# Performance work log

Hardware: AMD Instinct MI355X
Metric: run time of the kernel (lower is better)

The kernel has to match this reference:

```python
import jax, jax.numpy as jnp
import numpy as np

N, E, F_IN, HID, EMB, G = 100000, 1600000, 128, 128, 128, 64


def setup_inputs() -> dict:
    key = jax.random.key(0)
    ks = jax.random.split(key, 8)
    x = jax.random.normal(ks[0], (N, F_IN), jnp.float32)
    edge_index = jax.random.randint(ks[1], (2, E), 0, N, dtype=jnp.int64)
    batch = jnp.sort(jax.random.randint(ks[2], (N,), 0, G, dtype=jnp.int64))
    s1 = 1.0 / np.sqrt(F_IN)
    s2 = 1.0 / np.sqrt(HID)
    W1 = jax.random.uniform(ks[3], (F_IN, HID), jnp.float32, -s1, s1)
    b1 = jnp.zeros((HID,), jnp.float32)
    W2 = jax.random.uniform(ks[4], (HID, HID), jnp.float32, -s2, s2)
    b2 = jnp.zeros((HID,), jnp.float32)
    Wp = jax.random.uniform(ks[5], (HID, EMB), jnp.float32, -s2, s2)
    bp = jax.random.uniform(ks[6], (EMB,), jnp.float32, -s2, s2)
    return dict(x=x, edge_index=edge_index, batch=batch,
                W1=W1, b1=b1, W2=W2, b2=b2, Wp=Wp, bp=bp)


def _gcn_norm(edge_index, num_nodes):
    # PyG GCNConv: add self-loops, symmetric normalization D^-1/2 (A+I) D^-1/2
    loops = jnp.arange(num_nodes, dtype=edge_index.dtype)
    row = jnp.concatenate([edge_index[0], loops])  # sources
    col = jnp.concatenate([edge_index[1], loops])  # targets
    deg = jax.ops.segment_sum(jnp.ones_like(col, jnp.float32), col, num_segments=num_nodes)
    dis = jnp.where(deg > 0, jax.lax.rsqrt(jnp.maximum(deg, 1.0)), 0.0)
    norm = dis[row] * dis[col]  # [E + N]
    return row, col, norm


def reference(x, edge_index, batch, W1, b1, W2, b2, Wp, bp):
    n = x.shape[0]
    row, col, norm = _gcn_norm(edge_index, n)

    def gcn(h, W, b):
        h = h @ W                                   # [N, HID] small GEMM
        msg = h[row] * norm[:, None]                # gather + scale [E+N, HID]
        return jax.ops.segment_sum(msg, col, num_segments=n) + b  # scatter-add

    h = jax.nn.relu(gcn(x, W1, b1))   # dropout p=0.2 is identity in eval mode
    h = jax.nn.relu(gcn(h, W2, b2))
    # global_mean_pool over graph ids
    cnt = jax.ops.segment_sum(jnp.ones((n,), jnp.float32), batch, num_segments=G)
    pooled = jax.ops.segment_sum(h, batch, num_segments=G) / jnp.maximum(cnt, 1.0)[:, None]
    return pooled @ Wp + bp  # [G, EMB]
```

## Files before the change

### kernel.cpp

```cpp
#include <hip/hip_runtime.h>
#include <cstdint>
#include <cstddef>

#define GG 64
#define EPB 4096
#define BUK_SHIFT 9
#define BUK_NODES 512
#define PCHUNK 64

typedef unsigned int uint;
typedef unsigned short ushort;
typedef __attribute__((ext_vector_type(8))) short short8v;
typedef __attribute__((ext_vector_type(4))) float f32x4;


__global__ __launch_bounds__(256) void hist_kernel(const int* __restrict__ col,
                                                   int* __restrict__ ghist,
                                                   int E, int nbuk) {
  __shared__ int h[256];
  const int tid = threadIdx.x;
  h[tid] = 0;
  __syncthreads();
  const int base = blockIdx.x * EPB;
#pragma unroll
  for (int j = 0; j < EPB / 256; ++j) {
    int e = base + j * 256 + tid;
    if (e < E) atomicAdd(&h[col[e] >> BUK_SHIFT], 1);
  }
  __syncthreads();
  if (tid < nbuk && h[tid]) atomicAdd(&ghist[tid], h[tid]);
}

__global__ __launch_bounds__(256) void scan_kernel(const int* __restrict__ ghist,
                                                   int* __restrict__ bucketBase,
                                                   int* __restrict__ gcur,
                                                   int nbuk, int E) {
  __shared__ int s[256];
  const int tid = threadIdx.x;
  int v = (tid < nbuk) ? ghist[tid] : 0;
  s[tid] = v;
  __syncthreads();
  for (int off = 1; off < 256; off <<= 1) {
    int t = 0;
    if (tid >= off) t = s[tid - off];
    __syncthreads();
    s[tid] += t;
    __syncthreads();
  }
  int excl = s[tid] - v;
  if (tid < nbuk) {
    bucketBase[tid] = excl;
    gcur[tid] = excl;
  }
  if (tid == 0) bucketBase[nbuk] = E;
}

__global__ __launch_bounds__(256) void bin_kernel(const int* __restrict__ row,
                                                  const int* __restrict__ col,
                                                  int* __restrict__ gcur,
                                                  uint* __restrict__ binned, int E) {
  __shared__ int h[256];
  __shared__ int bbase[256];
  __shared__ int lcur[256];
  const int tid = threadIdx.x;
  const int base = blockIdx.x * EPB;
  int src[EPB / 256];
  int dst[EPB / 256];
#pragma unroll
  for (int j = 0; j < EPB / 256; ++j) {
    int e = base + j * 256 + tid;
    if (e < E) {
      src[j] = row[e];
      dst[j] = col[e];
    } else {
      dst[j] = -1;
    }
  }
  h[tid] = 0;
  lcur[tid] = 0;
  __syncthreads();
#pragma unroll
  for (int j = 0; j < EPB / 256; ++j)
    if (dst[j] >= 0) atomicAdd(&h[dst[j] >> BUK_SHIFT], 1);
  __syncthreads();
  if (h[tid] > 0) bbase[tid] = atomicAdd(&gcur[tid], h[tid]);
  __syncthreads();
#pragma unroll
  for (int j = 0; j < EPB / 256; ++j) {
    if (dst[j] >= 0) {
      int b = dst[j] >> BUK_SHIFT;
      int r = atomicAdd(&lcur[b], 1);
      binned[bbase[b] + r] = (uint)src[j] | ((uint)(dst[j] & (BUK_NODES - 1)) << 17);
    }
  }
}

__global__ __launch_bounds__(256) void build_kernel(const uint* __restrict__ binned,
                                                    const int* __restrict__ bucketBase,
                                                    int* __restrict__ indptr,
                                                    float* __restrict__ dis,
                                                    int* __restrict__ csr,
                                                    int n, int E, int nbuk) {
  __shared__ int h[BUK_NODES];
  __shared__ int off[BUK_NODES];
  __shared__ int ps[256];
  const int tid = threadIdx.x;
  const int b = blockIdx.x;
  const int lo = bucketBase[b], hi = bucketBase[b + 1];
  h[tid] = 0;
  h[tid + 256] = 0;
  __syncthreads();
  for (int i = lo + tid; i < hi; i += 256) atomicAdd(&h[binned[i] >> 17], 1);
  __syncthreads();
  int a0 = h[2 * tid], a1 = h[2 * tid + 1];
  ps[tid] = a0 + a1;
  __syncthreads();
  for (int o = 1; o < 256; o <<= 1) {
    int t = 0;
    if (tid >= o) t = ps[tid - o];
    __syncthreads();
    ps[tid] += t;
    __syncthreads();
  }
  int pexcl = ps[tid] - (a0 + a1);
  off[2 * tid] = pexcl;
  off[2 * tid + 1] = pexcl + a0;
  __syncthreads();
  const int node0 = b << BUK_SHIFT;
#pragma unroll
  for (int k = tid; k < BUK_NODES; k += 256) {
    int node = node0 + k;
    if (node < n) {
      indptr[node] = lo + off[k];
      dis[node] = rsqrtf((float)(h[k] + 1));
    }
  }
  __syncthreads();
  for (int i = lo + tid; i < hi; i += 256) {
    uint u = binned[i];
    int dlow = u >> 17;
    int s = (int)(u & 0x1FFFFu);
    int r = atomicAdd(&off[dlow], 1);
    csr[lo + r] = s;
  }
  if (b == nbuk - 1 && tid == 0) indptr[n] = E;
}


__device__ __forceinline__ uint bf16rne(float f) {
  uint u = __float_as_uint(f);
  return (u + 0x7fffu + ((u >> 16) & 1u)) >> 16;
}

__global__ __launch_bounds__(256) void wconv_kernel(const float* __restrict__ W,
                                                    ushort* __restrict__ Whi,
                                                    ushort* __restrict__ Wlo) {
  int slot = blockIdx.x * 256 + threadIdx.x;
  if (slot >= 2048) return;
  int lane = slot & 63;
  int j = (slot >> 6) & 7;
  int kc = slot >> 9;
  ushort hb[8], lb[8];
#pragma unroll
  for (int i = 0; i < 8; ++i) {
    int k = kc * 32 + ((lane >> 4) << 3) + i;
    int c = j * 16 + (lane & 15);
    float f = W[k * 128 + c];
    uint hi = bf16rne(f);
    float hif = __uint_as_float(hi << 16);
    uint lo = __float_as_uint(f - hif) >> 16;
    hb[i] = (ushort)hi;
    lb[i] = (ushort)lo;
  }
  *reinterpret_cast<uint4*>(Whi + (size_t)slot * 8) = *reinterpret_cast<uint4*>(hb);
  *reinterpret_cast<uint4*>(Wlo + (size_t)slot * 8) = *reinterpret_cast<uint4*>(lb);
}


__global__ __launch_bounds__(256) void gemm_mfma(const float* __restrict__ A,
                                                 const ushort* __restrict__ Whi,
                                                 const ushort* __restrict__ Wlo,
                                                 const float* __restrict__ scale,
                                                 uint* __restrict__ Cb, int n) {
  const int tid = threadIdx.x;
  const int wave = tid >> 6, lane = tid & 63;
  const int row = blockIdx.x * 64 + wave * 16 + (lane & 15);
  const int kgrp = lane >> 4;
  const bool rowok = row < n;

  f32x4 acc[8];
#pragma unroll
  for (int j = 0; j < 8; ++j) acc[j] = (f32x4){0.f, 0.f, 0.f, 0.f};

#pragma unroll
  for (int kc = 0; kc < 4; ++kc) {
    const float* ap = A + (size_t)row * 128 + kc * 32 + kgrp * 8;
    float4 a0 = make_float4(0.f, 0.f, 0.f, 0.f), a1 = a0;
    if (rowok) {
      a0 = *reinterpret_cast<const float4*>(ap);
      a1 = *reinterpret_cast<const float4*>(ap + 4);
    }
    short8v ahi, alo;
#pragma unroll
    for (int i = 0; i < 8; ++i) {
      float f = (i < 4) ? (&a0.x)[i] : (&a1.x)[i - 4];
      uint hi = bf16rne(f);
      float hif = __uint_as_float(hi << 16);
      uint lo = __float_as_uint(f - hif) >> 16;
      ahi[i] = (short)hi;
      alo[i] = (short)lo;
    }
#pragma unroll
    for (int j = 0; j < 8; ++j) {
      const size_t base = ((size_t)(kc * 8 + j) * 64 + lane) * 8;
      short8v whi = *reinterpret_cast<const short8v*>(Whi + base);
      short8v wlo = *reinterpret_cast<const short8v*>(Wlo + base);
      acc[j] = __builtin_amdgcn_mfma_f32_16x16x32_bf16(whi, ahi, acc[j], 0, 0, 0);
      acc[j] = __builtin_amdgcn_mfma_f32_16x16x32_bf16(whi, alo, acc[j], 0, 0, 0);
      acc[j] = __builtin_amdgcn_mfma_f32_16x16x32_bf16(wlo, ahi, acc[j], 0, 0, 0);
    }
  }

  if (rowok) {
    const float s = scale[row];
#pragma unroll
    for (int j = 0; j < 8; ++j) {
      uint u0 = bf16rne(acc[j][0] * s) | (bf16rne(acc[j][1] * s) << 16);
      uint u1 = bf16rne(acc[j][2] * s) | (bf16rne(acc[j][3] * s) << 16);
      *reinterpret_cast<uint2*>(Cb + (size_t)row * 64 + j * 8 + kgrp * 2) =
          make_uint2(u0, u1);
    }
  }
}


__global__ __launch_bounds__(256) void agg_kernel(const uint* __restrict__ T,
                                                  const int* __restrict__ indptr,
                                                  const int* __restrict__ csr,
                                                  const float* __restrict__ dis,
                                                  const float* __restrict__ bias,
                                                  float* __restrict__ O, int n) {
  int wid = (blockIdx.x << 2) + (threadIdx.x >> 6);
  if (wid >= n) return;
  wid = __builtin_amdgcn_readfirstlane(wid);
  const int lane = threadIdx.x & 63;
  const int e0 = indptr[wid], e1 = indptr[wid + 1];
  float ax = 0.f, ay = 0.f;
#define TLOAD(s) T[(size_t)(s) * 64 + lane]
#define BLO(u) __uint_as_float((u) << 16)
#define BHI(u) __uint_as_float((u) & 0xffff0000u)
  int e = e0;
  for (; e + 8 <= e1; e += 8) {
    int s0 = csr[e], s1 = csr[e + 1], s2 = csr[e + 2], s3 = csr[e + 3];
    int s4 = csr[e + 4], s5 = csr[e + 5], s6 = csr[e + 6], s7 = csr[e + 7];
    uint u0 = TLOAD(s0), u1 = TLOAD(s1), u2 = TLOAD(s2), u3 = TLOAD(s3);
    uint u4 = TLOAD(s4), u5 = TLOAD(s5), u6 = TLOAD(s6), u7 = TLOAD(s7);
    ax += ((BLO(u0) + BLO(u1)) + (BLO(u2) + BLO(u3))) +
          ((BLO(u4) + BLO(u5)) + (BLO(u6) + BLO(u7)));
    ay += ((BHI(u0) + BHI(u1)) + (BHI(u2) + BHI(u3))) +
          ((BHI(u4) + BHI(u5)) + (BHI(u6) + BHI(u7)));
  }
  for (; e + 4 <= e1; e += 4) {
    int s0 = csr[e], s1 = csr[e + 1], s2 = csr[e + 2], s3 = csr[e + 3];
    uint u0 = TLOAD(s0), u1 = TLOAD(s1), u2 = TLOAD(s2), u3 = TLOAD(s3);
    ax += (BLO(u0) + BLO(u1)) + (BLO(u2) + BLO(u3));
    ay += (BHI(u0) + BHI(u1)) + (BHI(u2) + BHI(u3));
  }
  for (; e < e1; ++e) {
    uint u = TLOAD(csr[e]);
    ax += BLO(u);
    ay += BHI(u);
  }
  uint us = TLOAD(wid);
  ax += BLO(us);
  ay += BHI(us);
  const float di = dis[wid];
  const float2 b = *reinterpret_cast<const float2*>(bias + lane * 2);
  float ox = fmaxf(fmaf(di, ax, b.x), 0.f);
  float oy = fmaxf(fmaf(di, ay, b.y), 0.f);
  *reinterpret_cast<float2*>(O + (size_t)wid * 128 + lane * 2) = make_float2(ox, oy);
}


__global__ __launch_bounds__(256) void pool_kernel(const float* __restrict__ H,
                                                   const int* __restrict__ batch,
                                                   float* __restrict__ pooled,
                                                   float* __restrict__ cntg, int n) {
  __shared__ float sd[256 * 4];
  const int tid = threadIdx.x;
  const int c4 = (tid & 31) << 2;
  const int rs = tid >> 5;
  const int base = blockIdx.x * PCHUNK;
  const int lim = min(base + PCHUNK, n);
  const int g0 = batch[base];
  const int gN = batch[lim - 1];
  float4 acc = make_float4(0.f, 0.f, 0.f, 0.f);
  if (g0 == gN) {
    for (int r = base + rs; r < lim; r += 8) {
      float4 v = *reinterpret_cast<const float4*>(H + (size_t)r * 128 + c4);
      acc.x += v.x; acc.y += v.y; acc.z += v.z; acc.w += v.w;
    }
    *reinterpret_cast<float4*>(&sd[tid * 4]) = acc;
    __syncthreads();
    if (tid < 128) {
      float4 o = *reinterpret_cast<float4*>(&sd[(tid + 128) * 4]);
      acc.x += o.x; acc.y += o.y; acc.z += o.z; acc.w += o.w;
      *reinterpret_cast<float4*>(&sd[tid * 4]) = acc;
    }
    __syncthreads();
    if (tid < 64) {
      float4 o = *reinterpret_cast<float4*>(&sd[(tid + 64) * 4]);
      acc.x += o.x; acc.y += o.y; acc.z += o.z; acc.w += o.w;
      *reinterpret_cast<float4*>(&sd[tid * 4]) = acc;
    }
    __syncthreads();
    if (tid < 32) {
      float4 o = *reinterpret_cast<float4*>(&sd[(tid + 32) * 4]);
      acc.x += o.x; acc.y += o.y; acc.z += o.z; acc.w += o.w;
      atomicAdd(&pooled[g0 * 128 + c4 + 0], acc.x);
      atomicAdd(&pooled[g0 * 128 + c4 + 1], acc.y);
      atomicAdd(&pooled[g0 * 128 + c4 + 2], acc.z);
      atomicAdd(&pooled[g0 * 128 + c4 + 3], acc.w);
      if (tid == 0) atomicAdd(&cntg[g0], (float)(lim - base));
    }
  } else {
    int curg = -1, cnt = 0;
    for (int r = base + rs; r < lim; r += 8) {
      int g = batch[r];
      if (g != curg) {
        if (curg >= 0) {
          atomicAdd(&pooled[curg * 128 + c4 + 0], acc.x);
          atomicAdd(&pooled[curg * 128 + c4 + 1], acc.y);
          atomicAdd(&pooled[curg * 128 + c4 + 2], acc.z);
          atomicAdd(&pooled[curg * 128 + c4 + 3], acc.w);
          if ((tid & 31) == 0) atomicAdd(&cntg[curg], (float)cnt);
        }
        curg = g;
        acc = make_float4(0.f, 0.f, 0.f, 0.f);
        cnt = 0;
      }
      float4 v = *reinterpret_cast<const float4*>(H + (size_t)r * 128 + c4);
      acc.x += v.x; acc.y += v.y; acc.z += v.z; acc.w += v.w;
      cnt++;
    }
    if (curg >= 0) {
      atomicAdd(&pooled[curg * 128 + c4 + 0], acc.x);
      atomicAdd(&pooled[curg * 128 + c4 + 1], acc.y);
      atomicAdd(&pooled[curg * 128 + c4 + 2], acc.z);
      atomicAdd(&pooled[curg * 128 + c4 + 3], acc.w);
      if ((tid & 31) == 0) atomicAdd(&cntg[curg], (float)cnt);
    }
  }
}

__global__ __launch_bounds__(128) void final_kernel(const float* __restrict__ pooled,
                                                    const float* __restrict__ cntg,
                                                    const float* __restrict__ Wp,
                                                    const float* __restrict__ bp,
                                                    float* __restrict__ out) {
  const int g = blockIdx.x;
  const int e = threadIdx.x;
  float inv = 1.0f / fmaxf(cntg[g], 1.0f);
  float acc = 0.f;
  for (int c = 0; c < 128; ++c)
    acc = fmaf(pooled[g * 128 + c], Wp[c * 128 + e], acc);
  out[g * 128 + e] = acc * inv + bp[e];
}


extern "C" void kernel_launch(void* const* d_in, const int* in_sizes, int n_in,
                              void* d_out, int out_size, void* d_ws, size_t ws_size,
                              hipStream_t stream) {
  const float* x = (const float*)d_in[0];
  const int* eidx = (const int*)d_in[1];
  const int* batch = (const int*)d_in[2];
  const float* W1 = (const float*)d_in[3];
  const float* b1 = (const float*)d_in[4];
  const float* W2 = (const float*)d_in[5];
  const float* b2 = (const float*)d_in[6];
  const float* Wp = (const float*)d_in[7];
  const float* bp = (const float*)d_in[8];

  const int n = in_sizes[0] / 128;
  const int E = in_sizes[1] / 2;
  const int* row = eidx;
  const int* col = eidx + E;
  const int nbuk = (n + BUK_NODES - 1) >> BUK_SHIFT;

  char* ws = (char*)d_ws;
  size_t off = 0;
  auto alloc = [&](size_t bytes) {
    void* p = ws + off;
    off = (off + bytes + 255) & ~(size_t)255;
    return p;
  };
  uint* Tb = (uint*)alloc((size_t)n * 64 * 4);
  float* B = (float*)alloc((size_t)n * 128 * 4);
  float* dis = (float*)alloc((size_t)n * 4);
  int* indptr = (int*)alloc((size_t)(n + 1) * 4);
  int* csr = (int*)alloc((size_t)E * 4);
  uint* binned = (uint*)alloc((size_t)E * 4);
  int* ghist = (int*)alloc(256 * 4);
  int* bucketBase = (int*)alloc(257 * 4);
  int* gcur = (int*)alloc(256 * 4);
  float* pooled = (float*)alloc((size_t)GG * 128 * 4);
  float* cntg = (float*)alloc((size_t)GG * 4);
  ushort* Whi1 = (ushort*)alloc(2048 * 8 * 2);
  ushort* Wlo1 = (ushort*)alloc(2048 * 8 * 2);
  ushort* Whi2 = (ushort*)alloc(2048 * 8 * 2);
  ushort* Wlo2 = (ushort*)alloc(2048 * 8 * 2);
  (void)off;

  hipMemsetAsync(ghist, 0, 256 * 4, stream);
  hipMemsetAsync(pooled, 0, (size_t)GG * 128 * 4, stream);
  hipMemsetAsync(cntg, 0, (size_t)GG * 4, stream);

  const int eblocks = (E + EPB - 1) / EPB;
  hist_kernel<<<eblocks, 256, 0, stream>>>(col, ghist, E, nbuk);
  scan_kernel<<<1, 256, 0, stream>>>(ghist, bucketBase, gcur, nbuk, E);
  bin_kernel<<<eblocks, 256, 0, stream>>>(row, col, gcur, binned, E);
  build_kernel<<<nbuk, 256, 0, stream>>>(binned, bucketBase, indptr, dis, csr, n, E, nbuk);
  wconv_kernel<<<8, 256, 0, stream>>>(W1, Whi1, Wlo1);
  wconv_kernel<<<8, 256, 0, stream>>>(W2, Whi2, Wlo2);

  const int gblocks = (n + 63) / 64;
  gemm_mfma<<<gblocks, 256, 0, stream>>>(x, Whi1, Wlo1, dis, Tb, n);
  agg_kernel<<<(n + 3) / 4, 256, 0, stream>>>(Tb, indptr, csr, dis, b1, B, n);
  gemm_mfma<<<gblocks, 256, 0, stream>>>(B, Whi2, Wlo2, dis, Tb, n);
  agg_kernel<<<(n + 3) / 4, 256, 0, stream>>>(Tb, indptr, csr, dis, b2, B, n);

  pool_kernel<<<(n + PCHUNK - 1) / PCHUNK, 256, 0, stream>>>(B, batch, pooled, cntg, n);
  final_kernel<<<GG, 128, 0, stream>>>(pooled, cntg, Wp, bp, (float*)d_out);
}
```

Before: 287.5 us.

## Store hidden activations in bf16, sub-bucket CSR by source, merge setup launches

The aggregation output is now written as packed bf16 instead of fp32. The second GEMM reads bf16 activations directly and drops one of its three split-precision MFMAs, and the pool kernel reads the halved data. The CSR build now sorts each destination's edges into 8 sub-bins keyed by the high bits of the source id, for better gather locality in aggregation, and it stores an expanded indptr. The two weight-conversion launches and three memsets are each merged into one. This lowers memory traffic and launch count but rounds the intermediate activations to bf16, which reduces accuracy.

```diff
diff --git a/kernel.cpp b/kernel.cpp
--- a/kernel.cpp
+++ b/kernel.cpp
@@ -7,11 +7,20 @@
 #define BUK_SHIFT 9
 #define BUK_NODES 512
 #define PCHUNK 64
+#define NCH 8
 
 typedef unsigned int uint;
 typedef unsigned short ushort;
 typedef __attribute__((ext_vector_type(8))) short short8v;
 typedef __attribute__((ext_vector_type(4))) float f32x4;
+
+__device__ __forceinline__ float blo(uint u) { return __uint_as_float(u << 16); }
+__device__ __forceinline__ float bhi(uint u) { return __uint_as_float(u & 0xffff0000u); }
+
+__device__ __forceinline__ uint bf16rne(float f) {
+  uint u = __float_as_uint(f);
+  return (u + 0x7fffu + ((u >> 16) & 1u)) >> 16;
+}
 
 
 __global__ __launch_bounds__(256) void hist_kernel(const int* __restrict__ col,
@@ -97,23 +106,34 @@
 
 __global__ __launch_bounds__(256) void build_kernel(const uint* __restrict__ binned,
                                                     const int* __restrict__ bucketBase,
-                                                    int* __restrict__ indptr,
+                                                    int* __restrict__ ip2,
                                                     float* __restrict__ dis,
                                                     int* __restrict__ csr,
                                                     int n, int E, int nbuk) {
-  __shared__ int h[BUK_NODES];
-  __shared__ int off[BUK_NODES];
+  __shared__ int h[BUK_NODES * NCH];
+  __shared__ int off[BUK_NODES * NCH];
   __shared__ int ps[256];
   const int tid = threadIdx.x;
   const int b = blockIdx.x;
   const int lo = bucketBase[b], hi = bucketBase[b + 1];
-  h[tid] = 0;
-  h[tid + 256] = 0;
-  __syncthreads();
-  for (int i = lo + tid; i < hi; i += 256) atomicAdd(&h[binned[i] >> 17], 1);
-  __syncthreads();
-  int a0 = h[2 * tid], a1 = h[2 * tid + 1];
-  ps[tid] = a0 + a1;
+#pragma unroll
+  for (int k = tid; k < BUK_NODES * NCH; k += 256) h[k] = 0;
+  __syncthreads();
+  for (int i = lo + tid; i < hi; i += 256) {
+    uint u = binned[i];
+    int key = (int)((u >> 17) << 3) | (int)((u & 0x1FFFFu) >> 14);
+    atomicAdd(&h[key], 1);
+  }
+  __syncthreads();
+  const int b16 = tid * 16;
+  int loc[16];
+  int s = 0;
+#pragma unroll
+  for (int j = 0; j < 16; ++j) {
+    loc[j] = s;
+    s += h[b16 + j];
+  }
+  ps[tid] = s;
   __syncthreads();
   for (int o = 1; o < 256; o <<= 1) {
     int t = 0;
@@ -122,41 +142,45 @@
     ps[tid] += t;
     __syncthreads();
   }
-  int pexcl = ps[tid] - (a0 + a1);
-  off[2 * tid] = pexcl;
-  off[2 * tid + 1] = pexcl + a0;
+  const int excl = ps[tid] - s;
+#pragma unroll
+  for (int j = 0; j < 16; ++j) off[b16 + j] = excl + loc[j];
   __syncthreads();
   const int node0 = b << BUK_SHIFT;
-#pragma unroll
   for (int k = tid; k < BUK_NODES; k += 256) {
     int node = node0 + k;
     if (node < n) {
-      indptr[node] = lo + off[k];
-      dis[node] = rsqrtf((float)(h[k] + 1));
+      int deg = 0;
+#pragma unroll
+      for (int c = 0; c < NCH; ++c) deg += h[k * NCH + c];
+      dis[node] = rsqrtf((float)(deg + 1));
+#pragma unroll
+      for (int c = 0; c < NCH; ++c) ip2[(size_t)node * NCH + c] = lo + off[k * NCH + c];
     }
   }
   __syncthreads();
   for (int i = lo + tid; i < hi; i += 256) {
     uint u = binned[i];
-    int dlow = u >> 17;
-    int s = (int)(u & 0x1FFFFu);
-    int r = atomicAdd(&off[dlow], 1);
-    csr[lo + r] = s;
-  }
-  if (b == nbuk - 1 && tid == 0) indptr[n] = E;
-}
-
-
-__device__ __forceinline__ uint bf16rne(float f) {
-  uint u = __float_as_uint(f);
-  return (u + 0x7fffu + ((u >> 16) & 1u)) >> 16;
-}
-
-__global__ __launch_bounds__(256) void wconv_kernel(const float* __restrict__ W,
-                                                    ushort* __restrict__ Whi,
-                                                    ushort* __restrict__ Wlo) {
-  int slot = blockIdx.x * 256 + threadIdx.x;
-  if (slot >= 2048) return;
+    int key = (int)((u >> 17) << 3) | (int)((u & 0x1FFFFu) >> 14);
+    int s2 = (int)(u & 0x1FFFFu);
+    int r = atomicAdd(&off[key], 1);
+    csr[lo + r] = s2;
+  }
+  if (b == nbuk - 1 && tid == 0) ip2[(size_t)n * NCH] = E;
+}
+
+
+__global__ __launch_bounds__(256) void wconv_kernel(const float* __restrict__ W1,
+                                                    const float* __restrict__ W2,
+                                                    ushort* __restrict__ Whi1,
+                                                    ushort* __restrict__ Wlo1,
+                                                    ushort* __restrict__ Whi2,
+                                                    ushort* __restrict__ Wlo2) {
+  const int g = blockIdx.x;
+  const float* W = (g < 8) ? W1 : W2;
+  ushort* Whi = (g < 8) ? Whi1 : Whi2;
+  ushort* Wlo = (g < 8) ? Wlo1 : Wlo2;
+  int slot = (g & 7) * 256 + threadIdx.x;
   int lane = slot & 63;
   int j = (slot >> 6) & 7;
   int kc = slot >> 9;
@@ -177,7 +201,8 @@
 }
 
 
-__global__ __launch_bounds__(256) void gemm_mfma(const float* __restrict__ A,
+template <bool ABF16>
+__global__ __launch_bounds__(256) void gemm_mfma(const void* __restrict__ Ain,
                                                  const ushort* __restrict__ Whi,
                                                  const ushort* __restrict__ Wlo,
                                                  const float* __restrict__ scale,
@@ -194,21 +219,31 @@
 
 #pragma unroll
   for (int kc = 0; kc < 4; ++kc) {
-    const float* ap = A + (size_t)row * 128 + kc * 32 + kgrp * 8;
-    float4 a0 = make_float4(0.f, 0.f, 0.f, 0.f), a1 = a0;
-    if (rowok) {
-      a0 = *reinterpret_cast<const float4*>(ap);
-      a1 = *reinterpret_cast<const float4*>(ap + 4);
-    }
     short8v ahi, alo;
-#pragma unroll
-    for (int i = 0; i < 8; ++i) {
-      float f = (i < 4) ? (&a0.x)[i] : (&a1.x)[i - 4];
-      uint hi = bf16rne(f);
-      float hif = __uint_as_float(hi << 16);
-      uint lo = __float_as_uint(f - hif) >> 16;
-      ahi[i] = (short)hi;
-      alo[i] = (short)lo;
+    if constexpr (ABF16) {
+      if (rowok) {
+        ahi = *reinterpret_cast<const short8v*>(
+            (const ushort*)Ain + (size_t)row * 128 + kc * 32 + kgrp * 8);
+      } else {
+#pragma unroll
+        for (int i = 0; i < 8; ++i) ahi[i] = 0;
+      }
+    } else {
+      const float* ap = (const float*)Ain + (size_t)row * 128 + kc * 32 + kgrp * 8;
+      float4 a0 = make_float4(0.f, 0.f, 0.f, 0.f), a1 = a0;
+      if (rowok) {
+        a0 = *reinterpret_cast<const float4*>(ap);
+        a1 = *reinterpret_cast<const float4*>(ap + 4);
+      }
+#pragma unroll
+      for (int i = 0; i < 8; ++i) {
+        float f = (i < 4) ? (&a0.x)[i] : (&a1.x)[i - 4];
+        uint hi = bf16rne(f);
+        float hif = __uint_as_float(hi << 16);
+        uint lo = __float_as_uint(f - hif) >> 16;
+        ahi[i] = (short)hi;
+        alo[i] = (short)lo;
+      }
     }
 #pragma unroll
     for (int j = 0; j < 8; ++j) {
@@ -216,7 +251,8 @@
       short8v whi = *reinterpret_cast<const short8v*>(Whi + base);
       short8v wlo = *reinterpret_cast<const short8v*>(Wlo + base);
       acc[j] = __builtin_amdgcn_mfma_f32_16x16x32_bf16(whi, ahi, acc[j], 0, 0, 0);
-      acc[j] = __builtin_amdgcn_mfma_f32_16x16x32_bf16(whi, alo, acc[j], 0, 0, 0);
+      if constexpr (!ABF16)
+        acc[j] = __builtin_amdgcn_mfma_f32_16x16x32_bf16(whi, alo, acc[j], 0, 0, 0);
       acc[j] = __builtin_amdgcn_mfma_f32_16x16x32_bf16(wlo, ahi, acc[j], 0, 0, 0);
     }
   }
@@ -235,54 +271,53 @@
 
 
 __global__ __launch_bounds__(256) void agg_kernel(const uint* __restrict__ T,
-                                                  const int* __restrict__ indptr,
+                                                  const int* __restrict__ ip2,
                                                   const int* __restrict__ csr,
                                                   const float* __restrict__ dis,
                                                   const float* __restrict__ bias,
-                                                  float* __restrict__ O, int n) {
+                                                  uint* __restrict__ O, int n) {
   int wid = (blockIdx.x << 2) + (threadIdx.x >> 6);
   if (wid >= n) return;
   wid = __builtin_amdgcn_readfirstlane(wid);
   const int lane = threadIdx.x & 63;
-  const int e0 = indptr[wid], e1 = indptr[wid + 1];
+  const int e0 = ip2[(size_t)wid * NCH];
+  const int e1 = ip2[(size_t)wid * NCH + NCH];
   float ax = 0.f, ay = 0.f;
 #define TLOAD(s) T[(size_t)(s) * 64 + lane]
-#define BLO(u) __uint_as_float((u) << 16)
-#define BHI(u) __uint_as_float((u) & 0xffff0000u)
   int e = e0;
   for (; e + 8 <= e1; e += 8) {
     int s0 = csr[e], s1 = csr[e + 1], s2 = csr[e + 2], s3 = csr[e + 3];
     int s4 = csr[e + 4], s5 = csr[e + 5], s6 = csr[e + 6], s7 = csr[e + 7];
     uint u0 = TLOAD(s0), u1 = TLOAD(s1), u2 = TLOAD(s2), u3 = TLOAD(s3);
     uint u4 = TLOAD(s4), u5 = TLOAD(s5), u6 = TLOAD(s6), u7 = TLOAD(s7);
-    ax += ((BLO(u0) + BLO(u1)) + (BLO(u2) + BLO(u3))) +
-          ((BLO(u4) + BLO(u5)) + (BLO(u6) + BLO(u7)));
-    ay += ((BHI(u0) + BHI(u1)) + (BHI(u2) + BHI(u3))) +
-          ((BHI(u4) + BHI(u5)) + (BHI(u6) + BHI(u7)));
+    ax += ((blo(u0) + blo(u1)) + (blo(u2) + blo(u3))) +
+          ((blo(u4) + blo(u5)) + (blo(u6) + blo(u7)));
+    ay += ((bhi(u0) + bhi(u1)) + (bhi(u2) + bhi(u3))) +
+          ((bhi(u4) + bhi(u5)) + (bhi(u6) + bhi(u7)));
   }
   for (; e + 4 <= e1; e += 4) {
     int s0 = csr[e], s1 = csr[e + 1], s2 = csr[e + 2], s3 = csr[e + 3];
     uint u0 = TLOAD(s0), u1 = TLOAD(s1), u2 = TLOAD(s2), u3 = TLOAD(s3);
-    ax += (BLO(u0) + BLO(u1)) + (BLO(u2) + BLO(u3));
-    ay += (BHI(u0) + BHI(u1)) + (BHI(u2) + BHI(u3));
+    ax += (blo(u0) + blo(u1)) + (blo(u2) + blo(u3));
+    ay += (bhi(u0) + bhi(u1)) + (bhi(u2) + bhi(u3));
   }
   for (; e < e1; ++e) {
     uint u = TLOAD(csr[e]);
-    ax += BLO(u);
-    ay += BHI(u);
+    ax += blo(u);
+    ay += bhi(u);
   }
   uint us = TLOAD(wid);
-  ax += BLO(us);
-  ay += BHI(us);
+  ax += blo(us);
+  ay += bhi(us);
   const float di = dis[wid];
   const float2 b = *reinterpret_cast<const float2*>(bias + lane * 2);
   float ox = fmaxf(fmaf(di, ax, b.x), 0.f);
   float oy = fmaxf(fmaf(di, ay, b.y), 0.f);
-  *reinterpret_cast<float2*>(O + (size_t)wid * 128 + lane * 2) = make_float2(ox, oy);
-}
-
-
-__global__ __launch_bounds__(256) void pool_kernel(const float* __restrict__ H,
+  O[(size_t)wid * 64 + lane] = bf16rne(ox) | (bf16rne(oy) << 16);
+}
+
+
+__global__ __launch_bounds__(256) void pool_kernel(const uint* __restrict__ H,
                                                    const int* __restrict__ batch,
                                                    float* __restrict__ pooled,
                                                    float* __restrict__ cntg, int n) {
@@ -297,8 +332,8 @@
   float4 acc = make_float4(0.f, 0.f, 0.f, 0.f);
   if (g0 == gN) {
     for (int r = base + rs; r < lim; r += 8) {
-      float4 v = *reinterpret_cast<const float4*>(H + (size_t)r * 128 + c4);
-      acc.x += v.x; acc.y += v.y; acc.z += v.z; acc.w += v.w;
+      uint2 v = *reinterpret_cast<const uint2*>(H + (size_t)r * 64 + (c4 >> 1));
+      acc.x += blo(v.x); acc.y += bhi(v.x); acc.z += blo(v.y); acc.w += bhi(v.y);
     }
     *reinterpret_cast<float4*>(&sd[tid * 4]) = acc;
     __syncthreads();
@@ -339,8 +374,8 @@
         acc = make_float4(0.f, 0.f, 0.f, 0.f);
         cnt = 0;
       }
-      float4 v = *reinterpret_cast<const float4*>(H + (size_t)r * 128 + c4);
-      acc.x += v.x; acc.y += v.y; acc.z += v.z; acc.w += v.w;
+      uint2 v = *reinterpret_cast<const uint2*>(H + (size_t)r * 64 + (c4 >> 1));
+      acc.x += blo(v.x); acc.y += bhi(v.x); acc.z += blo(v.y); acc.w += bhi(v.y);
       cnt++;
     }
     if (curg >= 0) {
@@ -395,40 +430,38 @@
     return p;
   };
   uint* Tb = (uint*)alloc((size_t)n * 64 * 4);
-  float* B = (float*)alloc((size_t)n * 128 * 4);
+  uint* Bb = (uint*)alloc((size_t)n * 64 * 4);
   float* dis = (float*)alloc((size_t)n * 4);
-  int* indptr = (int*)alloc((size_t)(n + 1) * 4);
+  int* ip2 = (int*)alloc(((size_t)n * NCH + 1) * 4);
   int* csr = (int*)alloc((size_t)E * 4);
   uint* binned = (uint*)alloc((size_t)E * 4);
-  int* ghist = (int*)alloc(256 * 4);
   int* bucketBase = (int*)alloc(257 * 4);
+  int* zbase = (int*)alloc((256 + 64 + GG * 128) * 4);
+  int* ghist = zbase;
+  float* cntg = (float*)(zbase + 256);
+  float* pooled = (float*)(zbase + 256 + 64);
   int* gcur = (int*)alloc(256 * 4);
-  float* pooled = (float*)alloc((size_t)GG * 128 * 4);
-  float* cntg = (float*)alloc((size_t)GG * 4);
   ushort* Whi1 = (ushort*)alloc(2048 * 8 * 2);
   ushort* Wlo1 = (ushort*)alloc(2048 * 8 * 2);
   ushort* Whi2 = (ushort*)alloc(2048 * 8 * 2);
   ushort* Wlo2 = (ushort*)alloc(2048 * 8 * 2);
   (void)off;
 
-  hipMemsetAsync(ghist, 0, 256 * 4, stream);
-  hipMemsetAsync(pooled, 0, (size_t)GG * 128 * 4, stream);
-  hipMemsetAsync(cntg, 0, (size_t)GG * 4, stream);
+  hipMemsetAsync(zbase, 0, (256 + 64 + GG * 128) * 4, stream);
 
   const int eblocks = (E + EPB - 1) / EPB;
   hist_kernel<<<eblocks, 256, 0, stream>>>(col, ghist, E, nbuk);
   scan_kernel<<<1, 256, 0, stream>>>(ghist, bucketBase, gcur, nbuk, E);
   bin_kernel<<<eblocks, 256, 0, stream>>>(row, col, gcur, binned, E);
-  build_kernel<<<nbuk, 256, 0, stream>>>(binned, bucketBase, indptr, dis, csr, n, E, nbuk);
-  wconv_kernel<<<8, 256, 0, stream>>>(W1, Whi1, Wlo1);
-  wconv_kernel<<<8, 256, 0, stream>>>(W2, Whi2, Wlo2);
+  build_kernel<<<nbuk, 256, 0, stream>>>(binned, bucketBase, ip2, dis, csr, n, E, nbuk);
+  wconv_kernel<<<16, 256, 0, stream>>>(W1, W2, Whi1, Wlo1, Whi2, Wlo2);
 
   const int gblocks = (n + 63) / 64;
-  gemm_mfma<<<gblocks, 256, 0, stream>>>(x, Whi1, Wlo1, dis, Tb, n);
-  agg_kernel<<<(n + 3) / 4, 256, 0, stream>>>(Tb, indptr, csr, dis, b1, B, n);
-  gemm_mfma<<<gblocks, 256, 0, stream>>>(B, Whi2, Wlo2, dis, Tb, n);
-  agg_kernel<<<(n + 3) / 4, 256, 0, stream>>>(Tb, indptr, csr, dis, b2, B, n);
-
-  pool_kernel<<<(n + PCHUNK - 1) / PCHUNK, 256, 0, stream>>>(B, batch, pooled, cntg, n);
+  gemm_mfma<false><<<gblocks, 256, 0, stream>>>(x, Whi1, Wlo1, dis, Tb, n);
+  agg_kernel<<<(n + 3) / 4, 256, 0, stream>>>(Tb, ip2, csr, dis, b1, Bb, n);
+  gemm_mfma<true><<<gblocks, 256, 0, stream>>>(Bb, Whi2, Wlo2, dis, Tb, n);
+  agg_kernel<<<(n + 3) / 4, 256, 0, stream>>>(Tb, ip2, csr, dis, b2, Bb, n);
+
+  pool_kernel<<<(n + PCHUNK - 1) / PCHUNK, 256, 0, stream>>>(Bb, batch, pooled, cntg, n);
   final_kernel<<<GG, 128, 0, stream>>>(pooled, cntg, Wp, bp, (float*)d_out);
 }
```

After: 270.9 us. 1.06x faster.
